# Kernel tuning notes

Measured on AMD Instinct MI355X. Metric: run time of the kernel, lower is better.

## Reference

```python
import jax, jax.numpy as jnp
import numpy as np

B, T, C = 4, 2048, 1024
N_HEAD = 16
D_HEAD = C // N_HEAD


def setup_inputs() -> dict:
    key = jax.random.key(0)
    ks = jax.random.split(key, 5)
    s_in = 1.0 / np.sqrt(C)
    return {
        "x": jax.random.normal(ks[0], (B, T, C), dtype=jnp.float32),
        "Wqkv": jax.random.uniform(ks[1], (C, 3 * C), dtype=jnp.float32, minval=-s_in, maxval=s_in),
        "bqkv": jax.random.uniform(ks[2], (3 * C,), dtype=jnp.float32, minval=-s_in, maxval=s_in),
        "Wproj": jax.random.uniform(ks[3], (C, C), dtype=jnp.float32, minval=-s_in, maxval=s_in),
        "bproj": jax.random.uniform(ks[4], (C,), dtype=jnp.float32, minval=-s_in, maxval=s_in),
    }


def reference(x, Wqkv, bqkv, Wproj, bproj):
    b, t, c = x.shape
    qkv = x @ Wqkv + bqkv                      # [B,T,3C]
    q, k, v = jnp.split(qkv, 3, axis=2)
    # [B,T,H,Dh] -> [B,H,T,Dh]
    q = q.reshape(b, t, N_HEAD, D_HEAD).transpose(0, 2, 1, 3)
    k = k.reshape(b, t, N_HEAD, D_HEAD).transpose(0, 2, 1, 3)
    v = v.reshape(b, t, N_HEAD, D_HEAD).transpose(0, 2, 1, 3)
    scale = 1.0 / np.sqrt(D_HEAD).astype(np.float32)
    att = jnp.einsum("bhqd,bhkd->bhqk", q, k) * scale   # [B,H,T,T]
    causal = jnp.tril(jnp.ones((t, t), dtype=bool))
    att = jnp.where(causal, att, jnp.float32(-jnp.inf))
    att = jax.nn.softmax(att, axis=-1)
    y = jnp.einsum("bhqk,bhkd->bhqd", att, v)            # [B,H,T,Dh]
    y = y.transpose(0, 2, 1, 3).reshape(b, t, c)
    return y @ Wproj + bproj
```

## Files before the change

kernel.cpp:

```cpp
#include <hip/hip_runtime.h>

using u16 = unsigned short;
typedef __attribute__((ext_vector_type(8))) __bf16 bf16x8;
typedef __attribute__((ext_vector_type(4))) float f32x4;
typedef __attribute__((ext_vector_type(16))) float f32x16;
typedef __attribute__((ext_vector_type(4))) unsigned int u32x4;
typedef __attribute__((ext_vector_type(2))) unsigned int u32x2;

__device__ inline u16 f2bf(float f) {
    unsigned u = __float_as_uint(f);
    u += 0x7FFFu + ((u >> 16) & 1u);
    return (u16)(u >> 16);
}
__device__ inline unsigned pack2(float a, float b) {
    return (unsigned)f2bf(a) | ((unsigned)f2bf(b) << 16);
}
__device__ inline bf16x8 as_bf16x8(u32x4 v) {
    union { u32x4 u; bf16x8 b; } x; x.u = v; return x.b;
}
__device__ inline unsigned cvtpk(float lo, float hi) {
    unsigned w;
    asm("v_cvt_pk_bf16_f32 %0, %1, %2" : "=v"(w) : "v"(lo), "v"(hi));
    return w;
}
__device__ inline void gload_lds16(const void* g, void* l) {
    __builtin_amdgcn_global_load_lds(
        (const __attribute__((address_space(1))) void*)g,
        (__attribute__((address_space(3))) void*)l, 16, 0, 0);
}
__device__ inline void ring_barrier() {
    __builtin_amdgcn_sched_barrier(0);
    asm volatile("s_waitcnt lgkmcnt(0)" ::: "memory");
    __builtin_amdgcn_sched_barrier(0);
    __builtin_amdgcn_s_barrier();
    __builtin_amdgcn_sched_barrier(0);
}

__global__ __launch_bounds__(256) void xcast(const float* __restrict__ in,
                                             u16* __restrict__ out) {
    const size_t i = ((size_t)blockIdx.x * 256 + threadIdx.x) * 8;
    f32x4 a = *(const f32x4*)(in + i);
    f32x4 b = *(const f32x4*)(in + i + 4);
    u32x4 w;
    w[0] = pack2(a[0], a[1]); w[1] = pack2(a[2], a[3]);
    w[2] = pack2(b[0], b[1]); w[3] = pack2(b[2], b[3]);
    *(u32x4*)(out + i) = w;
}

__global__ __launch_bounds__(256) void tcast_f32(const float* __restrict__ in,
                                                 u16* __restrict__ out,
                                                 int R, int C) {
    __shared__ float tile[64][65];
    const int r0 = blockIdx.x * 64, c0 = blockIdx.y * 64;
    const int t = threadIdx.x;
    {
        const int r = t >> 2, cq = (t & 3) * 16;
        const float* src = in + (size_t)(r0 + r) * C + c0 + cq;
#pragma unroll
        for (int j = 0; j < 4; ++j) {
            f32x4 v = *(const f32x4*)(src + j * 4);
#pragma unroll
            for (int e = 0; e < 4; ++e) tile[r][cq + j * 4 + e] = v[e];
        }
    }
    __syncthreads();
    {
        const int c = t >> 2, rq = (t & 3) * 16;
        u32x4 w0, w1;
#pragma unroll
        for (int j = 0; j < 4; ++j) {
            w0[j] = pack2(tile[rq + 2 * j][c], tile[rq + 2 * j + 1][c]);
            w1[j] = pack2(tile[rq + 8 + 2 * j][c], tile[rq + 8 + 2 * j + 1][c]);
        }
        u16* dst = out + (size_t)(c0 + c) * R + r0 + rq;
        *(u32x4*)dst = w0;
        *(u32x4*)(dst + 8) = w1;
    }
}

template <int EPI>
__global__ __launch_bounds__(256) void gemm_kernel(const u16* __restrict__ A,
                                                   const u16* __restrict__ Bt,
                                                   const float* __restrict__ bias,
                                                   void* __restrict__ outp,
                                                   u16* __restrict__ vtp,
                                                   const int M, const int N, const int K) {
    __shared__ char lds[49152];
    const int t = threadIdx.x;
    const int l = t & 63, wid = t >> 6;
    const int wr = wid >> 1, wc = wid & 1;
    const int g = l >> 4, lr = l & 15;
    const int m0 = blockIdx.x * 128, n0 = blockIdx.y * 128;

    f32x4 acc[4][4];
#pragma unroll
    for (int i = 0; i < 4; ++i)
#pragma unroll
        for (int j = 0; j < 4; ++j)
#pragma unroll
            for (int e = 0; e < 4; ++e) acc[i][j][e] = 0.f;

    const size_t Kb2 = (size_t)K * 2;
    const size_t rowbA = (size_t)(m0 + wid * 16 + (l >> 2)) * Kb2 + (l & 3) * 16;
    const size_t rowbB = (size_t)(n0 + wid * 16 + (l >> 2)) * Kb2 + (l & 3) * 16;
    const int kn = K >> 5;

    auto STAGE = [&](int kk) {
        char* buf = lds + (kk % 3) * 16384;
        const size_t kb = (size_t)kk * 64;
#pragma unroll
        for (int j = 0; j < 2; ++j) {
            gload_lds16((const char*)A + rowbA + j * 64 * Kb2 + kb,
                        buf + j * 4096 + wid * 1024);
            gload_lds16((const char*)Bt + rowbB + j * 64 * Kb2 + kb,
                        buf + 8192 + j * 4096 + wid * 1024);
        }
    };

    STAGE(0); STAGE(1);
#pragma unroll 1
    for (int kk = 0; kk < kn; ++kk) {
        if (kk + 1 < kn) asm volatile("s_waitcnt vmcnt(4)" ::: "memory");
        else             asm volatile("s_waitcnt vmcnt(0)" ::: "memory");
        ring_barrier();
        if (kk + 2 < kn) STAGE(kk + 2);
        const char* As = lds + (kk % 3) * 16384;
        const char* Bs = As + 8192;
        bf16x8 a[4], b[4];
#pragma unroll
        for (int m = 0; m < 4; ++m) {
            const int row = wr * 64 + m * 16 + lr;
            a[m] = as_bf16x8(*(const u32x4*)(As + row * 64 + g * 16));
        }
#pragma unroll
        for (int n = 0; n < 4; ++n) {
            const int row = wc * 64 + n * 16 + lr;
            b[n] = as_bf16x8(*(const u32x4*)(Bs + row * 64 + g * 16));
        }
        __builtin_amdgcn_s_setprio(1);
#pragma unroll
        for (int m = 0; m < 4; ++m)
#pragma unroll
            for (int n = 0; n < 4; ++n)
                acc[m][n] = __builtin_amdgcn_mfma_f32_16x16x32_bf16(a[m], b[n], acc[m][n], 0, 0, 0);
        __builtin_amdgcn_s_setprio(0);
    }

    const float qsc = (EPI == 0 && n0 < 1024) ? 0.18033688f : 1.0f;
#pragma unroll
    for (int m = 0; m < 4; ++m) {
#pragma unroll
        for (int n = 0; n < 4; ++n) {
            const int colg = n0 + wc * 64 + n * 16 + lr;
            const float bv = bias[colg];
            if constexpr (EPI == 0) {
                const int sec = colg >> 10, c = colg & 1023;
                const int hh = c >> 6, dd = c & 63;
                if (sec == 2) {
                    const int rowg0 = m0 + wr * 64 + m * 16 + g * 4;
                    const int bb = rowg0 >> 11, tt = rowg0 & 2047;
                    u16 pk[4];
#pragma unroll
                    for (int r = 0; r < 4; ++r)
                        pk[r] = f2bf(acc[m][n][r] + bv);
                    u16* dst = vtp + (((size_t)(bb * 16 + hh) * 64 + dd) << 11) + tt;
                    unsigned w0 = (unsigned)pk[0] | ((unsigned)pk[1] << 16);
                    unsigned w1 = (unsigned)pk[2] | ((unsigned)pk[3] << 16);
                    u32x2 wv; wv[0] = w0; wv[1] = w1;
                    *(u32x2*)dst = wv;
                } else {
#pragma unroll
                    for (int r = 0; r < 4; ++r) {
                        const int rowg = m0 + wr * 64 + m * 16 + g * 4 + r;
                        const float v = (acc[m][n][r] + bv) * qsc;
                        const int bb = rowg >> 11, tt = rowg & 2047;
                        u16* dst = (u16*)outp;
                        dst[(size_t)sec * 8388608u +
                            (((size_t)(bb * 16 + hh) * 2048 + tt) << 6) + dd] = f2bf(v);
                    }
                }
            } else {
#pragma unroll
                for (int r = 0; r < 4; ++r) {
                    const int rowg = m0 + wr * 64 + m * 16 + g * 4 + r;
                    ((float*)outp)[(size_t)rowg * N + colg] = acc[m][n][r] + bv;
                }
            }
        }
    }
}

__global__ __launch_bounds__(256) void attn_kernel(const u16* __restrict__ Q,
                                                   const u16* __restrict__ K,
                                                   const u16* __restrict__ Vt,
                                                   u16* __restrict__ Y) {
    __shared__ char lds[32768];
    const int t = threadIdx.x;
    const int l = t & 63, w = t >> 6;
    const int q = l & 31, hi = l >> 5;
    const int id = (int)blockIdx.y * 16 + (int)blockIdx.x;
    const int p = 15 - (id >> 6);
    const int bh = id & 63;
    const char* Kby = (const char*)(K + (size_t)bh * 131072);
    const char* Vby = (const char*)(Vt + (size_t)bh * 131072);
    const u16* Qb = Q + (size_t)bh * 131072;
    const int bb = bh >> 4, hh = bh & 15;
    const unsigned ck = (unsigned)(((l & 7) ^ (l >> 3)) << 4);
    const unsigned rd_swz = (unsigned)((q & 7) << 4);

    const int q0w = p * 128 + w * 32;
    const int qg = q0w + q;
    const int NT = 2 * p + 2;
    const int ntw = ((q0w + 31) >> 6) + 1;

    bf16x8 qf[4];
#pragma unroll
    for (int ks = 0; ks < 4; ++ks)
        qf[ks] = as_bf16x8(*(const u32x4*)(Qb + (size_t)(q0w + q) * 64 + ks * 16 + hi * 8));

    f32x16 o0, o1;
#pragma unroll
    for (int r = 0; r < 16; ++r) { o0[r] = 0.f; o1[r] = 0.f; }
    float lacc = 0.f;

    auto STAGE = [&](int it) {
        const int kv0 = it << 6;
        char* base = lds + (it & 1) * 16384;
#pragma unroll
        for (int j = 0; j < 2; ++j) {
            const int r = w * 16 + j * 8 + (l >> 3);
            gload_lds16(Kby + (size_t)(kv0 + r) * 128 + ck,
                        base + w * 2048 + j * 1024);
            gload_lds16(Vby + (size_t)r * 4096 + (size_t)kv0 * 2 + ck,
                        base + 8192 + w * 2048 + j * 1024);
        }
    };

    STAGE(0);
#pragma unroll 1
    for (int it = 0; it < NT; ++it) {
        asm volatile("s_waitcnt vmcnt(0)" ::: "memory");
        ring_barrier();
        if (it + 1 < NT) STAGE(it + 1);
        if (it < ntw) {
            const int kv0 = it << 6;
            const char* Kl = lds + (it & 1) * 16384;
            const char* Vl = Kl + 8192;
            u32x4 vf[8];
#pragma unroll
            for (int kvb = 0; kvb < 2; ++kvb)
#pragma unroll
                for (int s = 0; s < 2; ++s)
#pragma unroll
                    for (int db = 0; db < 2; ++db)
                        vf[kvb * 4 + s * 2 + db] = *(const u32x4*)(
                            Vl + (unsigned)((db * 32 + q) * 128) +
                            ((unsigned)(kvb * 64 + s * 32 + hi * 16) ^ rd_swz));
            f32x16 s0, s1;
#pragma unroll
            for (int r = 0; r < 16; ++r) { s0[r] = 0.f; s1[r] = 0.f; }
            __builtin_amdgcn_s_setprio(1);
#pragma unroll
            for (int ks = 0; ks < 4; ++ks) {
                const unsigned co = (unsigned)(ks * 32 + hi * 16) ^ rd_swz;
                bf16x8 kf0 = as_bf16x8(*(const u32x4*)(Kl + (unsigned)(q * 128) + co));
                s0 = __builtin_amdgcn_mfma_f32_32x32x16_bf16(kf0, qf[ks], s0, 0, 0, 0);
                bf16x8 kf1 = as_bf16x8(*(const u32x4*)(Kl + (unsigned)((32 + q) * 128) + co));
                s1 = __builtin_amdgcn_mfma_f32_32x32x16_bf16(kf1, qf[ks], s1, 0, 0, 0);
            }
            __builtin_amdgcn_s_setprio(0);
            if (kv0 + 63 > q0w) {
#pragma unroll
                for (int r = 0; r < 16; ++r) {
                    const int roff = (r & 3) + 8 * (r >> 2) + hi * 4;
                    if (kv0 + roff > qg) s0[r] = -1.0e30f;
                    if (kv0 + 32 + roff > qg) s1[r] = -1.0e30f;
                }
            }
            float sm[8];
#pragma unroll
            for (int j = 0; j < 8; ++j) {
                s0[2 * j]     = exp2f(s0[2 * j]);
                s0[2 * j + 1] = exp2f(s0[2 * j + 1]);
                s1[2 * j]     = exp2f(s1[2 * j]);
                s1[2 * j + 1] = exp2f(s1[2 * j + 1]);
                sm[j] = (s0[2 * j] + s0[2 * j + 1]) + (s1[2 * j] + s1[2 * j + 1]);
            }
            lacc += ((sm[0] + sm[1]) + (sm[2] + sm[3])) +
                    ((sm[4] + sm[5]) + (sm[6] + sm[7]));
#pragma unroll
            for (int kvb = 0; kvb < 2; ++kvb) {
                unsigned wd[8];
#pragma unroll
                for (int j = 0; j < 8; ++j) {
                    const float plo = kvb ? s1[2 * j] : s0[2 * j];
                    const float phi = kvb ? s1[2 * j + 1] : s0[2 * j + 1];
                    wd[j] = cvtpk(plo, phi);
                }
                u32x2 r0 = __builtin_amdgcn_permlane32_swap(wd[0], wd[2], false, false);
                u32x2 r1 = __builtin_amdgcn_permlane32_swap(wd[1], wd[3], false, false);
                u32x2 r2 = __builtin_amdgcn_permlane32_swap(wd[4], wd[6], false, false);
                u32x2 r3 = __builtin_amdgcn_permlane32_swap(wd[5], wd[7], false, false);
                u32x4 fa, fb;
                fa[0] = r0[0]; fa[1] = r1[0]; fa[2] = r0[1]; fa[3] = r1[1];
                fb[0] = r2[0]; fb[1] = r3[0]; fb[2] = r2[1]; fb[3] = r3[1];
                const bf16x8 pa = as_bf16x8(fa), pb = as_bf16x8(fb);
                __builtin_amdgcn_s_setprio(1);
                o0 = __builtin_amdgcn_mfma_f32_32x32x16_bf16(pa, as_bf16x8(vf[kvb * 4 + 0]), o0, 0, 0, 0);
                o1 = __builtin_amdgcn_mfma_f32_32x32x16_bf16(pa, as_bf16x8(vf[kvb * 4 + 1]), o1, 0, 0, 0);
                o0 = __builtin_amdgcn_mfma_f32_32x32x16_bf16(pb, as_bf16x8(vf[kvb * 4 + 2]), o0, 0, 0, 0);
                o1 = __builtin_amdgcn_mfma_f32_32x32x16_bf16(pb, as_bf16x8(vf[kvb * 4 + 3]), o1, 0, 0, 0);
                __builtin_amdgcn_s_setprio(0);
            }
        }
    }
    float lsum;
    {
        u32x2 rr = __builtin_amdgcn_permlane32_swap(
            __float_as_uint(lacc), __float_as_uint(lacc), false, false);
        lsum = lacc + __uint_as_float(hi ? rr[0] : rr[1]);
    }
    const float linv = 1.f / lsum;
#pragma unroll
    for (int r = 0; r < 16; ++r) {
        const int roff = (r & 3) + 8 * (r >> 2) + hi * 4;
        const float invq = __shfl(linv, roff);
        const size_t base = ((size_t)(bb * 2048 + q0w + roff)) * 1024 + hh * 64 + q;
        Y[base] = f2bf(o0[r] * invq);
        Y[base + 32] = f2bf(o1[r] * invq);
    }
}

extern "C" void kernel_launch(void* const* d_in, const int* in_sizes, int n_in,
                              void* d_out, int out_size, void* d_ws, size_t ws_size,
                              hipStream_t stream) {
    const float* x = (const float*)d_in[0];
    const float* Wqkv = (const float*)d_in[1];
    const float* bqkv = (const float*)d_in[2];
    const float* Wproj = (const float*)d_in[3];
    const float* bproj = (const float*)d_in[4];
    float* out = (float*)d_out;
    char* ws = (char*)d_ws;

    u16* Wtq = (u16*)(ws + 0);
    u16* Wtp = (u16*)(ws + 6291456);
    u16* Qb  = (u16*)(ws + 8388608);
    u16* Yb  = (u16*)(ws + 41943040);
    u16* Vtb = (u16*)(ws + 58720256);
    u16* Xb  = (u16*)(ws + 75497472);

    xcast<<<4096, 256, 0, stream>>>(x, Xb);
    tcast_f32<<<dim3(16, 48), 256, 0, stream>>>(Wqkv, Wtq, 1024, 3072);
    tcast_f32<<<dim3(16, 16), 256, 0, stream>>>(Wproj, Wtp, 1024, 1024);
    gemm_kernel<0><<<dim3(64, 24), 256, 0, stream>>>(
        Xb, Wtq, bqkv, (void*)Qb, Vtb, 8192, 3072, 1024);
    attn_kernel<<<dim3(16, 64), 256, 0, stream>>>(
        Qb, Qb + 8388608, Vtb, Yb);
    gemm_kernel<1><<<dim3(64, 8), 256, 0, stream>>>(
        Yb, Wtp, bproj, (void*)out, nullptr, 8192, 1024, 1024);
}
```

Measured before the change: 184.3 us.

## Load K and V fragments directly from global memory instead of LDS staging

Removes the double-buffered LDS staging of K/V tiles, along with the per-iteration waitcnt and block barrier. Each wave now reads its K and V MFMA fragments straight from global memory and loops only over its own causal tile count. This drops barrier synchronisation and lets waves run independently. In exchange, the four waves of a block each fetch the same K/V data from cache instead of sharing one LDS copy, and global load latency is no longer hidden by prefetching.

```diff
diff --git a/kernel.cpp b/kernel.cpp
--- a/kernel.cpp
+++ b/kernel.cpp
@@ -194,23 +194,19 @@
                                                    const u16* __restrict__ K,
                                                    const u16* __restrict__ Vt,
                                                    u16* __restrict__ Y) {
-    __shared__ char lds[32768];
     const int t = threadIdx.x;
     const int l = t & 63, w = t >> 6;
     const int q = l & 31, hi = l >> 5;
     const int id = (int)blockIdx.y * 16 + (int)blockIdx.x;
     const int p = 15 - (id >> 6);
     const int bh = id & 63;
-    const char* Kby = (const char*)(K + (size_t)bh * 131072);
-    const char* Vby = (const char*)(Vt + (size_t)bh * 131072);
+    const u16* Kb = K + (size_t)bh * 131072;
+    const u16* Vb = Vt + (size_t)bh * 131072;
     const u16* Qb = Q + (size_t)bh * 131072;
     const int bb = bh >> 4, hh = bh & 15;
-    const unsigned ck = (unsigned)(((l & 7) ^ (l >> 3)) << 4);
-    const unsigned rd_swz = (unsigned)((q & 7) << 4);
 
     const int q0w = p * 128 + w * 32;
     const int qg = q0w + q;
-    const int NT = 2 * p + 2;
     const int ntw = ((q0w + 31) >> 6) + 1;
 
     bf16x8 qf[4];
@@ -223,95 +219,74 @@
     for (int r = 0; r < 16; ++r) { o0[r] = 0.f; o1[r] = 0.f; }
     float lacc = 0.f;
 
-    auto STAGE = [&](int it) {
+#pragma unroll 1
+    for (int it = 0; it < ntw; ++it) {
         const int kv0 = it << 6;
-        char* base = lds + (it & 1) * 16384;
-#pragma unroll
-        for (int j = 0; j < 2; ++j) {
-            const int r = w * 16 + j * 8 + (l >> 3);
-            gload_lds16(Kby + (size_t)(kv0 + r) * 128 + ck,
-                        base + w * 2048 + j * 1024);
-            gload_lds16(Vby + (size_t)r * 4096 + (size_t)kv0 * 2 + ck,
-                        base + 8192 + w * 2048 + j * 1024);
-        }
-    };
-
-    STAGE(0);
-#pragma unroll 1
-    for (int it = 0; it < NT; ++it) {
-        asm volatile("s_waitcnt vmcnt(0)" ::: "memory");
-        ring_barrier();
-        if (it + 1 < NT) STAGE(it + 1);
-        if (it < ntw) {
-            const int kv0 = it << 6;
-            const char* Kl = lds + (it & 1) * 16384;
-            const char* Vl = Kl + 8192;
-            u32x4 vf[8];
-#pragma unroll
-            for (int kvb = 0; kvb < 2; ++kvb)
-#pragma unroll
-                for (int s = 0; s < 2; ++s)
-#pragma unroll
-                    for (int db = 0; db < 2; ++db)
-                        vf[kvb * 4 + s * 2 + db] = *(const u32x4*)(
-                            Vl + (unsigned)((db * 32 + q) * 128) +
-                            ((unsigned)(kvb * 64 + s * 32 + hi * 16) ^ rd_swz));
-            f32x16 s0, s1;
-#pragma unroll
-            for (int r = 0; r < 16; ++r) { s0[r] = 0.f; s1[r] = 0.f; }
+        u32x4 vf[8];
+#pragma unroll
+        for (int kvb = 0; kvb < 2; ++kvb)
+#pragma unroll
+            for (int s = 0; s < 2; ++s)
+#pragma unroll
+                for (int db = 0; db < 2; ++db)
+                    vf[kvb * 4 + s * 2 + db] = *(const u32x4*)(
+                        Vb + (size_t)(db * 32 + q) * 2048 + kv0 + kvb * 32 + s * 16 + hi * 8);
+        f32x16 s0, s1;
+#pragma unroll
+        for (int r = 0; r < 16; ++r) { s0[r] = 0.f; s1[r] = 0.f; }
+        __builtin_amdgcn_s_setprio(1);
+#pragma unroll
+        for (int ks = 0; ks < 4; ++ks) {
+            bf16x8 kf0 = as_bf16x8(*(const u32x4*)(
+                Kb + (size_t)(kv0 + q) * 64 + ks * 16 + hi * 8));
+            s0 = __builtin_amdgcn_mfma_f32_32x32x16_bf16(kf0, qf[ks], s0, 0, 0, 0);
+            bf16x8 kf1 = as_bf16x8(*(const u32x4*)(
+                Kb + (size_t)(kv0 + 32 + q) * 64 + ks * 16 + hi * 8));
+            s1 = __builtin_amdgcn_mfma_f32_32x32x16_bf16(kf1, qf[ks], s1, 0, 0, 0);
+        }
+        __builtin_amdgcn_s_setprio(0);
+        if (kv0 + 63 > q0w) {
+#pragma unroll
+            for (int r = 0; r < 16; ++r) {
+                const int roff = (r & 3) + 8 * (r >> 2) + hi * 4;
+                if (kv0 + roff > qg) s0[r] = -1.0e30f;
+                if (kv0 + 32 + roff > qg) s1[r] = -1.0e30f;
+            }
+        }
+        float sm[8];
+#pragma unroll
+        for (int j = 0; j < 8; ++j) {
+            s0[2 * j]     = exp2f(s0[2 * j]);
+            s0[2 * j + 1] = exp2f(s0[2 * j + 1]);
+            s1[2 * j]     = exp2f(s1[2 * j]);
+            s1[2 * j + 1] = exp2f(s1[2 * j + 1]);
+            sm[j] = (s0[2 * j] + s0[2 * j + 1]) + (s1[2 * j] + s1[2 * j + 1]);
+        }
+        lacc += ((sm[0] + sm[1]) + (sm[2] + sm[3])) +
+                ((sm[4] + sm[5]) + (sm[6] + sm[7]));
+#pragma unroll
+        for (int kvb = 0; kvb < 2; ++kvb) {
+            unsigned wd[8];
+#pragma unroll
+            for (int j = 0; j < 8; ++j) {
+                const float plo = kvb ? s1[2 * j] : s0[2 * j];
+                const float phi = kvb ? s1[2 * j + 1] : s0[2 * j + 1];
+                wd[j] = cvtpk(plo, phi);
+            }
+            u32x2 r0 = __builtin_amdgcn_permlane32_swap(wd[0], wd[2], false, false);
+            u32x2 r1 = __builtin_amdgcn_permlane32_swap(wd[1], wd[3], false, false);
+            u32x2 r2 = __builtin_amdgcn_permlane32_swap(wd[4], wd[6], false, false);
+            u32x2 r3 = __builtin_amdgcn_permlane32_swap(wd[5], wd[7], false, false);
+            u32x4 fa, fb;
+            fa[0] = r0[0]; fa[1] = r1[0]; fa[2] = r0[1]; fa[3] = r1[1];
+            fb[0] = r2[0]; fb[1] = r3[0]; fb[2] = r2[1]; fb[3] = r3[1];
+            const bf16x8 pa = as_bf16x8(fa), pb = as_bf16x8(fb);
             __builtin_amdgcn_s_setprio(1);
-#pragma unroll
-            for (int ks = 0; ks < 4; ++ks) {
-                const unsigned co = (unsigned)(ks * 32 + hi * 16) ^ rd_swz;
-                bf16x8 kf0 = as_bf16x8(*(const u32x4*)(Kl + (unsigned)(q * 128) + co));
-                s0 = __builtin_amdgcn_mfma_f32_32x32x16_bf16(kf0, qf[ks], s0, 0, 0, 0);
-                bf16x8 kf1 = as_bf16x8(*(const u32x4*)(Kl + (unsigned)((32 + q) * 128) + co));
-                s1 = __builtin_amdgcn_mfma_f32_32x32x16_bf16(kf1, qf[ks], s1, 0, 0, 0);
-            }
+            o0 = __builtin_amdgcn_mfma_f32_32x32x16_bf16(pa, as_bf16x8(vf[kvb * 4 + 0]), o0, 0, 0, 0);
+            o1 = __builtin_amdgcn_mfma_f32_32x32x16_bf16(pa, as_bf16x8(vf[kvb * 4 + 1]), o1, 0, 0, 0);
+            o0 = __builtin_amdgcn_mfma_f32_32x32x16_bf16(pb, as_bf16x8(vf[kvb * 4 + 2]), o0, 0, 0, 0);
+            o1 = __builtin_amdgcn_mfma_f32_32x32x16_bf16(pb, as_bf16x8(vf[kvb * 4 + 3]), o1, 0, 0, 0);
             __builtin_amdgcn_s_setprio(0);
-            if (kv0 + 63 > q0w) {
-#pragma unroll
-                for (int r = 0; r < 16; ++r) {
-                    const int roff = (r & 3) + 8 * (r >> 2) + hi * 4;
-                    if (kv0 + roff > qg) s0[r] = -1.0e30f;
-                    if (kv0 + 32 + roff > qg) s1[r] = -1.0e30f;
-                }
-            }
-            float sm[8];
-#pragma unroll
-            for (int j = 0; j < 8; ++j) {
-                s0[2 * j]     = exp2f(s0[2 * j]);
-                s0[2 * j + 1] = exp2f(s0[2 * j + 1]);
-                s1[2 * j]     = exp2f(s1[2 * j]);
-                s1[2 * j + 1] = exp2f(s1[2 * j + 1]);
-                sm[j] = (s0[2 * j] + s0[2 * j + 1]) + (s1[2 * j] + s1[2 * j + 1]);
-            }
-            lacc += ((sm[0] + sm[1]) + (sm[2] + sm[3])) +
-                    ((sm[4] + sm[5]) + (sm[6] + sm[7]));
-#pragma unroll
-            for (int kvb = 0; kvb < 2; ++kvb) {
-                unsigned wd[8];
-#pragma unroll
-                for (int j = 0; j < 8; ++j) {
-                    const float plo = kvb ? s1[2 * j] : s0[2 * j];
-                    const float phi = kvb ? s1[2 * j + 1] : s0[2 * j + 1];
-                    wd[j] = cvtpk(plo, phi);
-                }
-                u32x2 r0 = __builtin_amdgcn_permlane32_swap(wd[0], wd[2], false, false);
-                u32x2 r1 = __builtin_amdgcn_permlane32_swap(wd[1], wd[3], false, false);
-                u32x2 r2 = __builtin_amdgcn_permlane32_swap(wd[4], wd[6], false, false);
-                u32x2 r3 = __builtin_amdgcn_permlane32_swap(wd[5], wd[7], false, false);
-                u32x4 fa, fb;
-                fa[0] = r0[0]; fa[1] = r1[0]; fa[2] = r0[1]; fa[3] = r1[1];
-                fb[0] = r2[0]; fb[1] = r3[0]; fb[2] = r2[1]; fb[3] = r3[1];
-                const bf16x8 pa = as_bf16x8(fa), pb = as_bf16x8(fb);
-                __builtin_amdgcn_s_setprio(1);
-                o0 = __builtin_amdgcn_mfma_f32_32x32x16_bf16(pa, as_bf16x8(vf[kvb * 4 + 0]), o0, 0, 0, 0);
-                o1 = __builtin_amdgcn_mfma_f32_32x32x16_bf16(pa, as_bf16x8(vf[kvb * 4 + 1]), o1, 0, 0, 0);
-                o0 = __builtin_amdgcn_mfma_f32_32x32x16_bf16(pb, as_bf16x8(vf[kvb * 4 + 2]), o0, 0, 0, 0);
-                o1 = __builtin_amdgcn_mfma_f32_32x32x16_bf16(pb, as_bf16x8(vf[kvb * 4 + 3]), o1, 0, 0, 0);
-                __builtin_amdgcn_s_setprio(0);
-            }
         }
     }
     float lsum;
```

Result: slower. 258.2 us (+40.1%).
